# Optimization experiments

Measured on AMD Instinct MI355X. Metric: run time of the kernel, lower is better.

Reference implementation:

```python
import jax, jax.numpy as jnp
import numpy as np

B, P, H, D, CLASSES, L = 2048, 1024, 2048, 256, 10, 10
EP = 1e-64
LOG2PI = float(np.log(2.0 * np.pi))


def setup_inputs() -> dict:
    key = jax.random.key(0)
    ks = jax.random.split(key, 16)
    s = 0.05
    return {
        "data": jax.random.normal(ks[0], (B, P), dtype=jnp.float32),
        "mask": jax.random.randint(ks[1], (B, P), 0, 2) > 0,
        "enc_w1": jax.random.normal(ks[2], (P, H), dtype=jnp.float32) * s,
        "enc_b1": jnp.zeros((H,), jnp.float32),
        "enc_w2": jax.random.normal(ks[3], (H, 2 * D), dtype=jnp.float32) * s,
        "enc_b2": jnp.zeros((2 * D,), jnp.float32),
        "dec_w1": jax.random.normal(ks[4], (D, H), dtype=jnp.float32) * s,
        "dec_b1": jnp.zeros((H,), jnp.float32),
        "dec_w2": jax.random.normal(ks[5], (H, 3 * P), dtype=jnp.float32) * s,
        "dec_b2": jnp.zeros((3 * P,), jnp.float32),
        "cls_w1": jax.random.normal(ks[6], (P, H), dtype=jnp.float32) * s,
        "cls_b1": jnp.zeros((H,), jnp.float32),
        "cls_w2": jax.random.normal(ks[7], (H, CLASSES), dtype=jnp.float32) * s,
        "cls_b2": jnp.zeros((CLASSES,), jnp.float32),
    }


def _student_t_logprob(x, loc, scale, df):
    y = (x - loc) / scale
    return (jax.lax.lgamma((df + 1.0) * 0.5) - jax.lax.lgamma(df * 0.5)
            - 0.5 * jnp.log(df * jnp.pi) - jnp.log(scale)
            - 0.5 * (df + 1.0) * jnp.log1p(y * y / df))


def reference(data, mask, enc_w1, enc_b1, enc_w2, enc_b2,
              dec_w1, dec_b1, dec_w2, dec_b2,
              cls_w1, cls_b1, cls_w2, cls_b2):
    maskf = mask.astype(data.dtype)
    key = jax.random.key(42)
    k_eps, k_t = jax.random.split(key)

    # encoder
    he = jax.nn.relu(data @ enc_w1 + enc_b1)
    out_enc = he @ enc_w2 + enc_b2                      # [B, 2D]
    mu, sig = out_enc[:, :D], jax.nn.softplus(out_enc[:, D:]) + EP

    # reparameterized q(z|x) samples, L draws
    eps = jax.random.normal(k_eps, (L, B, D), dtype=data.dtype)
    z = mu[None] + sig[None] * eps                      # [L, B, D]
    zf = z.reshape(L * B, D)

    # decoder -> StudentT params
    hd = jax.nn.relu(zf @ dec_w1 + dec_b1)
    out_dec = hd @ dec_w2 + dec_b2                      # [L*B, 3P]
    means = out_dec[:, :P]
    scales = jax.nn.softplus(out_dec[:, P:2 * P]) + 0.001
    dfree = jax.nn.softplus(out_dec[:, 2 * P:]) + 3.0

    data_t = jnp.tile(data, (L, 1))                     # [L*B, P]
    mask_t = jnp.tile(maskf, (L, 1))
    logpx = _student_t_logprob(data_t, means, scales, dfree)
    logpxobs = jnp.sum(logpx * mask_t, axis=1).reshape(L, B)

    logpz = jnp.sum(-0.5 * z * z, axis=-1) - 0.5 * D * LOG2PI          # [L, B]
    logq = jnp.sum(-0.5 * eps * eps - jnp.log(sig)[None], axis=-1) - 0.5 * D * LOG2PI

    imp_w = jax.nn.softmax(logpxobs + logpz - logq, axis=0)            # [L, B]

    # non-reparameterized StudentT sample (torch .sample() is detached)
    t = jax.random.t(k_t, dfree, shape=dfree.shape)
    xms = jax.lax.stop_gradient(means + scales * t).reshape(L, B, P)
    xm = jnp.einsum('ki,kij->ij', imp_w, xms)

    data_imputed = jnp.where(mask, data, xm)
    hc = jax.nn.relu(data_imputed @ cls_w1 + cls_b1)
    logits = hc @ cls_w2 + cls_b2
    return (data_imputed, logits)
```

## Files before the change

### kernel.cpp

```cpp
#include <hip/hip_runtime.h>
#include <math.h>

typedef unsigned int u32;
typedef unsigned short u16;
typedef __attribute__((ext_vector_type(8))) short bf16x8;
typedef __attribute__((ext_vector_type(16))) float f32x16;

struct U2 { u32 a, b; };

__host__ __device__ __forceinline__ U2 tf2x32(u32 k0, u32 k1, u32 c0, u32 c1) {
  u32 ks2 = k0 ^ k1 ^ 0x1BD11BDAu;
  u32 x0 = c0 + k0, x1 = c1 + k1;
#define TFR(r) { x0 += x1; x1 = (x1 << (r)) | (x1 >> (32 - (r))); x1 ^= x0; }
  TFR(13) TFR(15) TFR(26) TFR(6)
  x0 += k1; x1 += ks2 + 1u;
  TFR(17) TFR(29) TFR(16) TFR(24)
  x0 += ks2; x1 += k0 + 2u;
  TFR(13) TFR(15) TFR(26) TFR(6)
  x0 += k0; x1 += k1 + 3u;
  TFR(17) TFR(29) TFR(16) TFR(24)
  x0 += k1; x1 += ks2 + 4u;
  TFR(13) TFR(15) TFR(26) TFR(6)
  x0 += ks2; x1 += k0 + 5u;
#undef TFR
  return {x0, x1};
}

__host__ __device__ __forceinline__ u32 prf32(u32 k0, u32 k1, u32 i) {
  U2 r = tf2x32(k0, k1, 0u, i);
  return r.a ^ r.b;
}

__device__ __forceinline__ float u01_from_bits(u32 bits) {
  u32 r = (bits >> 9) | 0x3f800000u;
  return __uint_as_float(r) - 1.0f;
}

__device__ __forceinline__ float erfinv_f32(float x) {
  float w = -log1pf(-x * x);
  float p;
  if (w < 5.0f) {
    w -= 2.5f;
    p = 2.81022636e-08f;
    p = fmaf(p, w, 3.43273939e-07f);
    p = fmaf(p, w, -3.5233877e-06f);
    p = fmaf(p, w, -4.39150654e-06f);
    p = fmaf(p, w, 0.00021858087f);
    p = fmaf(p, w, -0.00125372503f);
    p = fmaf(p, w, -0.00417768164f);
    p = fmaf(p, w, 0.246640727f);
    p = fmaf(p, w, 1.50140941f);
  } else {
    w = sqrtf(w) - 3.0f;
    p = -0.000200214257f;
    p = fmaf(p, w, 0.000100950558f);
    p = fmaf(p, w, 0.00134934322f);
    p = fmaf(p, w, -0.00367342844f);
    p = fmaf(p, w, 0.00573950773f);
    p = fmaf(p, w, -0.0076224613f);
    p = fmaf(p, w, 0.00943887047f);
    p = fmaf(p, w, 1.00167406f);
    p = fmaf(p, w, 2.83297682f);
  }
  return p * x;
}

__device__ __forceinline__ float normal_from_bits(u32 bits) {
  const float lo = -0.99999994f;
  float u = u01_from_bits(bits) * 2.0f + lo;
  u = fmaxf(lo, u);
  return 1.41421356237f * erfinv_f32(u);
}

__device__ __forceinline__ float softplus_f(float x) {
  return fmaxf(x, 0.0f) + log1pf(expf(-fabsf(x)));
}

__device__ float gamma_sample(u32 k0, u32 k1, float alpha) {
  U2 kk = tf2x32(k0, k1, 0u, 0u);
  k0 = kk.a; k1 = kk.b;
  float d = alpha - 0.33333334f;
  float c = 0.33333334f / sqrtf(d);
  float X, V, U;
  do {
    U2 nk = tf2x32(k0, k1, 0u, 0u);
    U2 xk = tf2x32(k0, k1, 0u, 1u);
    U2 uk = tf2x32(k0, k1, 0u, 2u);
    k0 = nk.a; k1 = nk.b;
    u32 xk0 = xk.a, xk1 = xk.b;
    float x, v;
    do {
      U2 nxt = tf2x32(xk0, xk1, 0u, 0u);
      U2 sub = tf2x32(xk0, xk1, 0u, 1u);
      xk0 = nxt.a; xk1 = nxt.b;
      x = normal_from_bits(prf32(sub.a, sub.b, 0u));
      v = 1.0f + x * c;
    } while (v <= 0.0f);
    X = x * x;
    V = (v * v) * v;
    U = u01_from_bits(prf32(uk.a, uk.b, 0u));
  } while (U >= 1.0f - 0.0331f * (X * X) &&
           logf(U) >= 0.5f * X + d * ((1.0f - V) + logf(V)));
  return d * V;
}

__device__ __forceinline__ u16 f2bf(float f) {
  u32 u = __float_as_uint(f);
  u32 r = ((u >> 16) & 1u) + 0x7fffu;
  return (u16)((u + r) >> 16);
}
__device__ __forceinline__ float bf2f(u16 h) { return __uint_as_float(((u32)h) << 16); }

__device__ __forceinline__ void split2(float v, u16& h, u16& m) {
  h = f2bf(v);
  m = f2bf(v - bf2f(h));
}

#define GLOAD16(gp, lp) __builtin_amdgcn_global_load_lds( \
    (const __attribute__((address_space(1))) void*)(gp),  \
    (__attribute__((address_space(3))) void*)(lp), 16, 0, 0)

template<bool RELU, bool SIX>
__global__ __launch_bounds__(256, 3) void gemm_s3(const u16* __restrict__ A2,
                                                  const u16* __restrict__ B2T,
                                                  const float* __restrict__ bias,
                                                  float* __restrict__ Cf,
                                                  u16* __restrict__ C2,
                                                  int N, int kbits) {
  __shared__ u16 As[128 * 64];
  __shared__ u16 Bs[128 * 64];
  const int tid = threadIdx.x;
  const int l = tid & 63, w = tid >> 6;
  const int m0 = blockIdx.y * 128, n0 = blockIdx.x * 128;
  const int K2 = 2 << kbits;
  const int srow = l >> 3;
  const int scol = ((l & 7) ^ srow) << 3;
  const u16* agr[4]; const u16* bgr[4]; u16* al[4]; u16* bl[4];
#pragma unroll
  for (int j = 0; j < 4; ++j) {
    int r = w * 32 + j * 8 + srow;
    agr[j] = A2 + (size_t)(m0 + r) * K2 + scol;
    bgr[j] = B2T + (size_t)(n0 + r) * K2 + scol;
    al[j] = &As[(w * 4 + j) * 512];
    bl[j] = &Bs[(w * 4 + j) * 512];
  }
  f32x16 acc[2][2] = {};
  const int fr = l & 31;
  const int wm = w >> 1, wn = w & 1;
  const int swz = (l & 7) << 4;
  const int hk16 = (l >> 5) << 4;
  const int nk = 3 << (kbits - 6);
  const int kmask = (1 << kbits) - 1;
  for (int kt = 0; kt < nk; ++kt) {
    int vb = kt << 6;
    int s = vb >> kbits;
    int ko = vb & kmask;
    int ao = ((s >> 1) << kbits) + ko;
    int bo = ((s & 1) << kbits) + ko;
    __syncthreads();
#pragma unroll
    for (int j = 0; j < 4; ++j) {
      GLOAD16(agr[j] + ao, al[j]);
      GLOAD16(bgr[j] + bo, bl[j]);
    }
    __syncthreads();
#pragma unroll
    for (int ks = 0; ks < 4; ++ks) {
      bf16x8 af[2], bf[2];
#pragma unroll
      for (int mi = 0; mi < 2; ++mi) {
        int ar = wm * 64 + mi * 32 + fr;
        af[mi] = *(const bf16x8*)((const char*)As + ar * 128 + ((ks * 32 + hk16) ^ swz));
      }
#pragma unroll
      for (int ni = 0; ni < 2; ++ni) {
        int br = wn * 64 + ni * 32 + fr;
        bf[ni] = *(const bf16x8*)((const char*)Bs + br * 128 + ((ks * 32 + hk16) ^ swz));
      }
#pragma unroll
      for (int mi = 0; mi < 2; ++mi)
#pragma unroll
        for (int ni = 0; ni < 2; ++ni)
          acc[mi][ni] = __builtin_amdgcn_mfma_f32_32x32x16_bf16(af[mi], bf[ni], acc[mi][ni], 0, 0, 0);
    }
  }
#pragma unroll
  for (int mi = 0; mi < 2; ++mi)
#pragma unroll
  for (int ni = 0; ni < 2; ++ni) {
    int gcol = n0 + wn * 64 + ni * 32 + fr;
    float bsv = bias[gcol];
#pragma unroll
    for (int r = 0; r < 16; ++r) {
      int grow = m0 + wm * 64 + mi * 32 + (r & 3) + 8 * (r >> 2) + 4 * (l >> 5);
      float v = acc[mi][ni][r] + bsv;
      if (RELU) v = fmaxf(v, 0.0f);
      if (!SIX) {
        Cf[(size_t)grow * N + gcol] = v;
      } else {
        u16 h, mm; split2(v, h, mm);
        u16* q = C2 + (size_t)grow * 2 * N + gcol;
        q[0] = h; q[N] = mm;
      }
    }
  }
}

__global__ __launch_bounds__(256) void k_wconv(const float* __restrict__ W, u16* __restrict__ W2T,
                                               int K, int N) {
  __shared__ float t[64][65];
  const int k0 = blockIdx.y * 64, n0 = blockIdx.x * 64;
  const int tid = threadIdx.x;
  for (int i = tid; i < 4096; i += 256) {
    int kk = i >> 6, nn = i & 63;
    t[kk][nn] = W[(size_t)(k0 + kk) * N + (n0 + nn)];
  }
  __syncthreads();
  const int nn = tid >> 2, kc = (tid & 3) << 4;
  u16* base = W2T + (size_t)(n0 + nn) * 2 * K + (k0 + kc);
#pragma unroll
  for (int kk = 0; kk < 16; ++kk) {
    u16 h, m; split2(t[kc + kk][nn], h, m);
    base[kk] = h; base[K + kk] = m;
  }
}

__global__ __launch_bounds__(256) void k_aconv(const float* __restrict__ X, u16* __restrict__ X2,
                                               int total, int kbits) {
  int i = blockIdx.x * 256 + threadIdx.x;
  if (i >= total) return;
  int K = 1 << kbits;
  int r = i >> kbits, k = i & (K - 1);
  u16 h, m; split2(X[i], h, m);
  u16* q = X2 + ((size_t)r * 2 << kbits) + k;
  q[0] = h; q[K] = m;
}

__global__ __launch_bounds__(256) void k_build(const int* __restrict__ mask,
                                               u16* __restrict__ miss,
                                               int* __restrict__ nmiss) {
  const int b = blockIdx.x, tid = threadIdx.x;
  const int* mrow = mask + b * 1024;
  const int pb = tid * 4;
  int m0 = (mrow[pb] == 0), m1 = (mrow[pb + 1] == 0),
      m2 = (mrow[pb + 2] == 0), m3 = (mrow[pb + 3] == 0);
  int cnt = m0 + m1 + m2 + m3;
  __shared__ int sc[256];
  sc[tid] = cnt;
  __syncthreads();
  for (int off = 1; off < 256; off <<= 1) {
    int v = 0;
    if (tid >= off) v = sc[tid - off];
    __syncthreads();
    sc[tid] += v;
    __syncthreads();
  }
  int pos = sc[tid] - cnt;
  u16* mr = miss + b * 1024;
  if (m0) mr[pos++] = (u16)pb;
  if (m1) mr[pos++] = (u16)(pb + 1);
  if (m2) mr[pos++] = (u16)(pb + 2);
  if (m3) mr[pos++] = (u16)(pb + 3);
  if (tid == 255) nmiss[b] = sc[255];
}

__global__ __launch_bounds__(256) void k_eps_z(const float* __restrict__ out_enc,
                                               u16* __restrict__ z2c,
                                               float* __restrict__ logpz,
                                               float* __restrict__ logq,
                                               int l0, u32 ke0, u32 ke1) {
  const int row = blockIdx.x;
  const int lb = l0 * 2048 + row;
  const int b = row & 2047;
  const int d = threadIdx.x;
  const u32 m = ((u32)lb << 8) + (u32)d;
  float mu = out_enc[b * 512 + d];
  float sg = softplus_f(out_enc[b * 512 + 256 + d]);
  float e = normal_from_bits(prf32(ke0, ke1, m));
  float zz = mu + sg * e;
  u16 h, mm; split2(zz, h, mm);
  u16* q = z2c + row * 512 + d;
  q[0] = h; q[256] = mm;
  float t1 = -0.5f * e * e - logf(sg);
  float t2 = -0.5f * zz * zz;
#pragma unroll
  for (int o = 32; o; o >>= 1) { t1 += __shfl_down(t1, o); t2 += __shfl_down(t2, o); }
  __shared__ float sm1[4], sm2[4];
  int lane = d & 63, wv = d >> 6;
  if (!lane) { sm1[wv] = t1; sm2[wv] = t2; }
  __syncthreads();
  if (d == 0) {
    float a = sm1[0] + sm1[1] + sm1[2] + sm1[3];
    float qq = sm2[0] + sm2[1] + sm2[2] + sm2[3];
    logq[lb]  = a - 235.2482645003962f;
    logpz[lb] = qq - 235.2482645003962f;
  }
}

__global__ __launch_bounds__(256) void k_lpx(const float* __restrict__ odec,
                                             const float* __restrict__ data,
                                             const int* __restrict__ mask,
                                             float* __restrict__ lpxobs,
                                             int l0) {
  const int row = blockIdx.x;
  const int lb = l0 * 2048 + row;
  const int b = row & 2047;
  const int tid = threadIdx.x;
  float lpsum = 0.0f;
  for (int j = 0; j < 4; ++j) {
    int p = tid + j * 256;
    if (mask[b * 1024 + p]) {
      float mean  = odec[(size_t)row * 3072 + p];
      float scale = softplus_f(odec[(size_t)row * 3072 + 1024 + p]) + 0.001f;
      float dfv   = softplus_f(odec[(size_t)row * 3072 + 2048 + p]) + 3.0f;
      float x = data[b * 1024 + p];
      float y = (x - mean) / scale;
      float lp = lgammaf((dfv + 1.0f) * 0.5f) - lgammaf(dfv * 0.5f)
               - 0.5f * logf(dfv * 3.14159274f) - logf(scale)
               - 0.5f * (dfv + 1.0f) * log1pf(y * y / dfv);
      lpsum += lp;
    }
  }
#pragma unroll
  for (int o = 32; o; o >>= 1) lpsum += __shfl_down(lpsum, o);
  __shared__ float sm[4];
  int lane = tid & 63, wv = tid >> 6;
  if (!lane) sm[wv] = lpsum;
  __syncthreads();
  if (tid == 0) lpxobs[lb] = sm[0] + sm[1] + sm[2] + sm[3];
}

__global__ __launch_bounds__(256) void k_sample(const float* __restrict__ odec,
                                                const u16* __restrict__ miss,
                                                const int* __restrict__ nmiss,
                                                u16* __restrict__ xms,
                                                int l0, u32 kn0, u32 kn1, u32 kg0, u32 kg1) {
  const int row = blockIdx.x;
  const int lb = l0 * 2048 + row;
  const int b = row & 2047;
  const int nm = nmiss[b];
  const u16* mr = miss + b * 1024;
  for (int t = threadIdx.x; t < nm; t += 256) {
    int p = mr[t];
    float mean  = odec[(size_t)row * 3072 + p];
    float scale = softplus_f(odec[(size_t)row * 3072 + 1024 + p]) + 0.001f;
    float dfv   = softplus_f(odec[(size_t)row * 3072 + 2048 + p]) + 3.0f;
    u32 i = ((u32)lb << 10) + (u32)p;
    float n = normal_from_bits(prf32(kn0, kn1, i));
    U2 gk = tf2x32(kg0, kg1, 0u, i);
    float half_df = dfv * 0.5f;
    float g = gamma_sample(gk.a, gk.b, half_df);
    float tt = n * sqrtf(half_df / g);
    xms[i] = f2bf(mean + scale * tt);
  }
}

__global__ __launch_bounds__(256) void k_impw(const float* __restrict__ lpx,
                                              const float* __restrict__ lpz,
                                              const float* __restrict__ lq,
                                              float* __restrict__ w) {
  int b = blockIdx.x * 256 + threadIdx.x;
  float s[10], mx = -INFINITY;
#pragma unroll
  for (int l = 0; l < 10; ++l) {
    s[l] = lpx[l * 2048 + b] + lpz[l * 2048 + b] - lq[l * 2048 + b];
    mx = fmaxf(mx, s[l]);
  }
  float se = 0.0f;
#pragma unroll
  for (int l = 0; l < 10; ++l) { s[l] = expf(s[l] - mx); se += s[l]; }
#pragma unroll
  for (int l = 0; l < 10; ++l) w[l * 2048 + b] = s[l] / se;
}

__global__ __launch_bounds__(256) void k_xm(const int* __restrict__ mask,
                                            const float* __restrict__ data,
                                            const float* __restrict__ impw,
                                            const u16* __restrict__ xms,
                                            u16* __restrict__ imp2,
                                            float* __restrict__ out) {
  int idx = blockIdx.x * 256 + threadIdx.x;
  int b = idx >> 10, p = idx & 1023;
  float o;
  if (mask[idx]) {
    o = data[idx];
  } else {
    float acc = 0.0f;
#pragma unroll
    for (int l = 0; l < 10; ++l)
      acc += impw[l * 2048 + b] * bf2f(xms[((size_t)l * 2048 + b) * 1024 + p]);
    o = acc;
  }
  out[idx] = o;
  u16 h, m; split2(o, h, m);
  u16* q = imp2 + (size_t)b * 2048 + p;
  q[0] = h; q[1024] = m;
}

__global__ __launch_bounds__(256) void k_cls2(const float* __restrict__ hc,
                                              const float* __restrict__ w2,
                                              const float* __restrict__ b2,
                                              float* __restrict__ out) {
  int b = blockIdx.x, tid = threadIdx.x;
  float acc[10];
#pragma unroll
  for (int c = 0; c < 10; ++c) acc[c] = 0.0f;
  for (int k = tid; k < 2048; k += 256) {
    float h = hc[(size_t)b * 2048 + k];
#pragma unroll
    for (int c = 0; c < 10; ++c) acc[c] = fmaf(h, w2[k * 10 + c], acc[c]);
  }
  __shared__ float red[4][10];
  int lane = tid & 63, wv = tid >> 6;
#pragma unroll
  for (int c = 0; c < 10; ++c) {
    float v = acc[c];
#pragma unroll
    for (int o = 32; o; o >>= 1) v += __shfl_down(v, o);
    if (!lane) red[wv][c] = v;
  }
  __syncthreads();
  if (tid < 10) out[b * 10 + tid] = red[0][tid] + red[1][tid] + red[2][tid] + red[3][tid] + b2[tid];
}

extern "C" void kernel_launch(void* const* d_in, const int* in_sizes, int n_in,
                              void* d_out, int out_size, void* d_ws, size_t ws_size,
                              hipStream_t stream) {
  const float* data   = (const float*)d_in[0];
  const int*   mask   = (const int*)d_in[1];
  const float* enc_w1 = (const float*)d_in[2];
  const float* enc_b1 = (const float*)d_in[3];
  const float* enc_w2 = (const float*)d_in[4];
  const float* enc_b2 = (const float*)d_in[5];
  const float* dec_w1 = (const float*)d_in[6];
  const float* dec_b1 = (const float*)d_in[7];
  const float* dec_w2 = (const float*)d_in[8];
  const float* dec_b2 = (const float*)d_in[9];
  const float* cls_w1 = (const float*)d_in[10];
  const float* cls_b1 = (const float*)d_in[11];
  const float* cls_w2 = (const float*)d_in[12];
  const float* cls_b2 = (const float*)d_in[13];

  float* out = (float*)d_out;
  char* wsb = (char*)d_ws;

  if (ws_size < 186982400ULL) return;

  u16*   xmsu   = (u16*)(wsb + 0);
  u16*   w_d2   = (u16*)(wsb + 41943040);
  u16*   w_d1   = (u16*)(wsb + 67108864);
  u16*   hx2    = (u16*)(wsb + 69206016);
  float* odec   = (float*)(wsb + 102760448);
  u16*   z2c    = (u16*)(wsb + 153092096);
  u16*   data2  = (u16*)(wsb + 157286400);
  u16*   w_ec   = (u16*)(wsb + 165675008);
  u16*   w_e2   = (u16*)(wsb + 174063616);
  float* logpz  = (float*)(wsb + 178257920);
  float* logq   = (float*)(wsb + 178339840);
  float* lpxobs = (float*)(wsb + 178421760);
  float* impw   = (float*)(wsb + 178503680);
  float* out_enc= (float*)(wsb + 178585600);
  u16*   miss   = (u16*)(wsb + 182779904);
  int*   nmiss  = (int*)(wsb + 186974208);
  float* hc     = odec;
  u16*   imp2   = data2;

  U2 ke = tf2x32(0u, 42u, 0u, 0u);
  U2 kt = tf2x32(0u, 42u, 0u, 1u);
  U2 kn = tf2x32(kt.a, kt.b, 0u, 0u);
  U2 kg = tf2x32(kt.a, kt.b, 0u, 1u);

  dim3 blk(256);
  k_aconv<<<8192, blk, 0, stream>>>(data, data2, 2097152, 10);
  k_wconv<<<dim3(32, 16), blk, 0, stream>>>(enc_w1, w_ec, 1024, 2048);
  k_wconv<<<dim3(8, 32),  blk, 0, stream>>>(enc_w2, w_e2, 2048, 512);
  k_wconv<<<dim3(48, 32), blk, 0, stream>>>(dec_w2, w_d2, 2048, 3072);
  k_wconv<<<dim3(32, 4),  blk, 0, stream>>>(dec_w1, w_d1, 256, 2048);
  k_build<<<2048, blk, 0, stream>>>(mask, miss, nmiss);

  gemm_s3<true,  true ><<<dim3(16, 16), blk, 0, stream>>>(data2, w_ec, enc_b1, nullptr, hx2, 2048, 10);
  gemm_s3<false, false><<<dim3(4, 16),  blk, 0, stream>>>(hx2, w_e2, enc_b2, out_enc, nullptr, 512, 11);

  for (int l0 = 0; l0 < 10; l0 += 2) {
    k_eps_z<<<4096, blk, 0, stream>>>(out_enc, z2c, logpz, logq, l0, ke.a, ke.b);
    gemm_s3<true,  true ><<<dim3(16, 32), blk, 0, stream>>>(z2c, w_d1, dec_b1, nullptr, hx2, 2048, 8);
    gemm_s3<false, false><<<dim3(24, 32), blk, 0, stream>>>(hx2, w_d2, dec_b2, odec, nullptr, 3072, 11);
    k_lpx<<<4096, blk, 0, stream>>>(odec, data, mask, lpxobs, l0);
    k_sample<<<4096, blk, 0, stream>>>(odec, miss, nmiss, xmsu, l0, kn.a, kn.b, kg.a, kg.b);
  }

  k_impw<<<8, blk, 0, stream>>>(lpxobs, logpz, logq, impw);
  k_xm<<<8192, blk, 0, stream>>>(mask, data, impw, xmsu, imp2, out);

  k_wconv<<<dim3(32, 16), blk, 0, stream>>>(cls_w1, w_ec, 1024, 2048);
  gemm_s3<true, false><<<dim3(16, 16), blk, 0, stream>>>(imp2, w_ec, cls_b1, hc, nullptr, 2048, 10);
  k_cls2<<<2048, blk, 0, stream>>>(hc, cls_w2, cls_b2, out + 2048 * 1024);
}
```

Measured before the change: 1.985 ms.

## Compact observed indices, cheaper lgamma difference, and defer gamma rejection retries

k_build now writes both the missing and the observed column indices per row, so k_lpx walks only the observed list and no longer has branch divergence on the mask. The lgamma difference lgamma((df+1)/2) - lgamma(df/2) is replaced by a closed-form shifted Stirling approximation. The gamma sampler does one Marsaglia-Tsang iteration inline, and rejected elements are pushed to a shared-memory queue and finished in a second pass, which compacts the retries and reduces warp divergence. The costs are extra LDS use, a shared atomic counter, and an approximation to lgamma that may differ slightly from lgammaf.

New measurement: 1.845 ms. 1.08x faster.

```diff
diff --git a/kernel.cpp b/kernel.cpp
--- a/kernel.cpp
+++ b/kernel.cpp
@@ -76,32 +76,38 @@
   return fmaxf(x, 0.0f) + log1pf(expf(-fabsf(x)));
 }
 
-__device__ float gamma_sample(u32 k0, u32 k1, float alpha) {
-  U2 kk = tf2x32(k0, k1, 0u, 0u);
-  k0 = kk.a; k1 = kk.b;
-  float d = alpha - 0.33333334f;
-  float c = 0.33333334f / sqrtf(d);
-  float X, V, U;
+struct GI { bool acc; float V; u32 k0, k1; };
+__device__ __forceinline__ GI gamma_iter(u32 k0, u32 k1, float d, float c) {
+  U2 nk = tf2x32(k0, k1, 0u, 0u);
+  U2 xk = tf2x32(k0, k1, 0u, 1u);
+  U2 uk = tf2x32(k0, k1, 0u, 2u);
+  u32 xk0 = xk.a, xk1 = xk.b;
+  float x, v;
   do {
-    U2 nk = tf2x32(k0, k1, 0u, 0u);
-    U2 xk = tf2x32(k0, k1, 0u, 1u);
-    U2 uk = tf2x32(k0, k1, 0u, 2u);
-    k0 = nk.a; k1 = nk.b;
-    u32 xk0 = xk.a, xk1 = xk.b;
-    float x, v;
-    do {
-      U2 nxt = tf2x32(xk0, xk1, 0u, 0u);
-      U2 sub = tf2x32(xk0, xk1, 0u, 1u);
-      xk0 = nxt.a; xk1 = nxt.b;
-      x = normal_from_bits(prf32(sub.a, sub.b, 0u));
-      v = 1.0f + x * c;
-    } while (v <= 0.0f);
-    X = x * x;
-    V = (v * v) * v;
-    U = u01_from_bits(prf32(uk.a, uk.b, 0u));
-  } while (U >= 1.0f - 0.0331f * (X * X) &&
-           logf(U) >= 0.5f * X + d * ((1.0f - V) + logf(V)));
-  return d * V;
+    U2 nxt = tf2x32(xk0, xk1, 0u, 0u);
+    U2 sub = tf2x32(xk0, xk1, 0u, 1u);
+    xk0 = nxt.a; xk1 = nxt.b;
+    x = normal_from_bits(prf32(sub.a, sub.b, 0u));
+    v = 1.0f + x * c;
+  } while (v <= 0.0f);
+  float X = x * x;
+  float V = (v * v) * v;
+  float U = u01_from_bits(prf32(uk.a, uk.b, 0u));
+  bool cont = (U >= 1.0f - 0.0331f * (X * X)) &&
+              (logf(U) >= 0.5f * X + d * ((1.0f - V) + logf(V)));
+  GI r; r.acc = !cont; r.V = V; r.k0 = nk.a; r.k1 = nk.b;
+  return r;
+}
+
+__device__ __forceinline__ float lgamma_half_diff(float x) {
+  float z = x + 3.0f;
+  float num = x * (x + 1.0f) * (x + 2.0f);
+  float den = (x + 0.5f) * (x + 1.5f) * (x + 2.5f);
+  float zh = z + 0.5f;
+  float iz = 1.0f / z, izh = 1.0f / zh;
+  float corr = 0.0833333333f * (izh - iz)
+             - 0.00277777778f * (izh * izh * izh - iz * iz * iz);
+  return logf(num / den) + 0.5f * logf(z) + z * log1pf(0.5f * iz) - 0.5f + corr;
 }
 
 __device__ __forceinline__ u16 f2bf(float f) {
@@ -237,7 +243,7 @@
 }
 
 __global__ __launch_bounds__(256) void k_build(const int* __restrict__ mask,
-                                               u16* __restrict__ miss,
+                                               u16* __restrict__ lists,
                                                int* __restrict__ nmiss) {
   const int b = blockIdx.x, tid = threadIdx.x;
   const int* mrow = mask + b * 1024;
@@ -256,12 +262,15 @@
     __syncthreads();
   }
   int pos = sc[tid] - cnt;
-  u16* mr = miss + b * 1024;
-  if (m0) mr[pos++] = (u16)pb;
-  if (m1) mr[pos++] = (u16)(pb + 1);
-  if (m2) mr[pos++] = (u16)(pb + 2);
-  if (m3) mr[pos++] = (u16)(pb + 3);
-  if (tid == 255) nmiss[b] = sc[255];
+  int nmT = sc[255];
+  u16* lr = lists + b * 1024;
+  int mpos = pos;
+  int opos = nmT + (pb - pos);
+  if (m0) lr[mpos++] = (u16)pb;       else lr[opos++] = (u16)pb;
+  if (m1) lr[mpos++] = (u16)(pb + 1); else lr[opos++] = (u16)(pb + 1);
+  if (m2) lr[mpos++] = (u16)(pb + 2); else lr[opos++] = (u16)(pb + 2);
+  if (m3) lr[mpos++] = (u16)(pb + 3); else lr[opos++] = (u16)(pb + 3);
+  if (tid == 255) nmiss[b] = nmT;
 }
 
 __global__ __launch_bounds__(256) void k_eps_z(const float* __restrict__ out_enc,
@@ -299,27 +308,29 @@
 
 __global__ __launch_bounds__(256) void k_lpx(const float* __restrict__ odec,
                                              const float* __restrict__ data,
-                                             const int* __restrict__ mask,
+                                             const u16* __restrict__ lists,
+                                             const int* __restrict__ nmiss,
                                              float* __restrict__ lpxobs,
                                              int l0) {
   const int row = blockIdx.x;
   const int lb = l0 * 2048 + row;
   const int b = row & 2047;
   const int tid = threadIdx.x;
+  const int nm = nmiss[b];
+  const u16* orow = lists + b * 1024 + nm;
+  const int no = 1024 - nm;
   float lpsum = 0.0f;
-  for (int j = 0; j < 4; ++j) {
-    int p = tid + j * 256;
-    if (mask[b * 1024 + p]) {
-      float mean  = odec[(size_t)row * 3072 + p];
-      float scale = softplus_f(odec[(size_t)row * 3072 + 1024 + p]) + 0.001f;
-      float dfv   = softplus_f(odec[(size_t)row * 3072 + 2048 + p]) + 3.0f;
-      float x = data[b * 1024 + p];
-      float y = (x - mean) / scale;
-      float lp = lgammaf((dfv + 1.0f) * 0.5f) - lgammaf(dfv * 0.5f)
-               - 0.5f * logf(dfv * 3.14159274f) - logf(scale)
-               - 0.5f * (dfv + 1.0f) * log1pf(y * y / dfv);
-      lpsum += lp;
-    }
+  for (int t = tid; t < no; t += 256) {
+    int p = orow[t];
+    float mean  = odec[(size_t)row * 3072 + p];
+    float scale = softplus_f(odec[(size_t)row * 3072 + 1024 + p]) + 0.001f;
+    float dfv   = softplus_f(odec[(size_t)row * 3072 + 2048 + p]) + 3.0f;
+    float x = data[b * 1024 + p];
+    float y = (x - mean) / scale;
+    float lp = lgamma_half_diff(dfv * 0.5f)
+             - 0.5f * logf(dfv * 3.14159274f) - logf(scale)
+             - 0.5f * (dfv + 1.0f) * log1pf(y * y / dfv);
+    lpsum += lp;
   }
 #pragma unroll
   for (int o = 32; o; o >>= 1) lpsum += __shfl_down(lpsum, o);
@@ -331,7 +342,7 @@
 }
 
 __global__ __launch_bounds__(256) void k_sample(const float* __restrict__ odec,
-                                                const u16* __restrict__ miss,
+                                                const u16* __restrict__ lists,
                                                 const int* __restrict__ nmiss,
                                                 u16* __restrict__ xms,
                                                 int l0, u32 kn0, u32 kn1, u32 kg0, u32 kg1) {
@@ -339,7 +350,12 @@
   const int lb = l0 * 2048 + row;
   const int b = row & 2047;
   const int nm = nmiss[b];
-  const u16* mr = miss + b * 1024;
+  const u16* mr = lists + b * 1024;
+  __shared__ u32 qk0[1024], qk1[1024];
+  __shared__ u16 qp[1024];
+  __shared__ int qn;
+  if (threadIdx.x == 0) qn = 0;
+  __syncthreads();
   for (int t = threadIdx.x; t < nm; t += 256) {
     int p = mr[t];
     float mean  = odec[(size_t)row * 3072 + p];
@@ -348,10 +364,36 @@
     u32 i = ((u32)lb << 10) + (u32)p;
     float n = normal_from_bits(prf32(kn0, kn1, i));
     U2 gk = tf2x32(kg0, kg1, 0u, i);
+    U2 kk = tf2x32(gk.a, gk.b, 0u, 0u);
     float half_df = dfv * 0.5f;
-    float g = gamma_sample(gk.a, gk.b, half_df);
-    float tt = n * sqrtf(half_df / g);
-    xms[i] = f2bf(mean + scale * tt);
+    float d = half_df - 0.33333334f;
+    float c = 0.33333334f / sqrtf(d);
+    GI r = gamma_iter(kk.a, kk.b, d, c);
+    if (r.acc) {
+      float g = d * r.V;
+      xms[i] = f2bf(mean + scale * (n * sqrtf(half_df / g)));
+    } else {
+      int s = atomicAdd(&qn, 1);
+      qk0[s] = r.k0; qk1[s] = r.k1; qp[s] = (u16)p;
+    }
+  }
+  __syncthreads();
+  int n2 = qn;
+  for (int t = threadIdx.x; t < n2; t += 256) {
+    int p = qp[t];
+    float mean  = odec[(size_t)row * 3072 + p];
+    float scale = softplus_f(odec[(size_t)row * 3072 + 1024 + p]) + 0.001f;
+    float dfv   = softplus_f(odec[(size_t)row * 3072 + 2048 + p]) + 3.0f;
+    u32 i = ((u32)lb << 10) + (u32)p;
+    float n = normal_from_bits(prf32(kn0, kn1, i));
+    float half_df = dfv * 0.5f;
+    float d = half_df - 0.33333334f;
+    float c = 0.33333334f / sqrtf(d);
+    u32 k0 = qk0[t], k1 = qk1[t];
+    GI r;
+    do { r = gamma_iter(k0, k1, d, c); k0 = r.k0; k1 = r.k1; } while (!r.acc);
+    float g = d * r.V;
+    xms[i] = f2bf(mean + scale * (n * sqrtf(half_df / g)));
   }
 }
 
@@ -460,7 +502,7 @@
   float* lpxobs = (float*)(wsb + 178421760);
   float* impw   = (float*)(wsb + 178503680);
   float* out_enc= (float*)(wsb + 178585600);
-  u16*   miss   = (u16*)(wsb + 182779904);
+  u16*   lists  = (u16*)(wsb + 182779904);
   int*   nmiss  = (int*)(wsb + 186974208);
   float* hc     = odec;
   u16*   imp2   = data2;
@@ -476,7 +518,7 @@
   k_wconv<<<dim3(8, 32),  blk, 0, stream>>>(enc_w2, w_e2, 2048, 512);
   k_wconv<<<dim3(48, 32), blk, 0, stream>>>(dec_w2, w_d2, 2048, 3072);
   k_wconv<<<dim3(32, 4),  blk, 0, stream>>>(dec_w1, w_d1, 256, 2048);
-  k_build<<<2048, blk, 0, stream>>>(mask, miss, nmiss);
+  k_build<<<2048, blk, 0, stream>>>(mask, lists, nmiss);
 
   gemm_s3<true,  true ><<<dim3(16, 16), blk, 0, stream>>>(data2, w_ec, enc_b1, nullptr, hx2, 2048, 10);
   gemm_s3<false, false><<<dim3(4, 16),  blk, 0, stream>>>(hx2, w_e2, enc_b2, out_enc, nullptr, 512, 11);
@@ -485,8 +527,8 @@
     k_eps_z<<<4096, blk, 0, stream>>>(out_enc, z2c, logpz, logq, l0, ke.a, ke.b);
     gemm_s3<true,  true ><<<dim3(16, 32), blk, 0, stream>>>(z2c, w_d1, dec_b1, nullptr, hx2, 2048, 8);
     gemm_s3<false, false><<<dim3(24, 32), blk, 0, stream>>>(hx2, w_d2, dec_b2, odec, nullptr, 3072, 11);
-    k_lpx<<<4096, blk, 0, stream>>>(odec, data, mask, lpxobs, l0);
-    k_sample<<<4096, blk, 0, stream>>>(odec, miss, nmiss, xmsu, l0, kn.a, kn.b, kg.a, kg.b);
+    k_lpx<<<4096, blk, 0, stream>>>(odec, data, lists, nmiss, lpxobs, l0);
+    k_sample<<<4096, blk, 0, stream>>>(odec, lists, nmiss, xmsu, l0, kn.a, kn.b, kg.a, kg.b);
   }
 
   k_impw<<<8, blk, 0, stream>>>(lpxobs, logpz, logq, impw);
```
